# Performance work log

Hardware: AMD Instinct MI355X
Metric: run time of the kernel (lower is better)

## Reference

```python
import jax, jax.numpy as jnp
import numpy as np

HIDDEN = 1024
HEADS = 16
HEAD_DIM = HIDDEN // HEADS  # 64
BATCH = 2
SEQ = 2048
MASK_IDENTITY = True


def setup_inputs() -> dict:
    key = jax.random.key(0)
    ks = jax.random.split(key, 9)
    s = 1.0 / np.sqrt(HIDDEN)
    return {
        "hidden_states": jax.random.normal(ks[0], (BATCH, SEQ, HIDDEN), jnp.float32),
        "Wq": jax.random.normal(ks[1], (HIDDEN, HIDDEN), jnp.float32) * s,
        "bq": jnp.zeros((HIDDEN,), jnp.float32),
        "Wk": jax.random.normal(ks[2], (HIDDEN, HIDDEN), jnp.float32) * s,
        "bk": jnp.zeros((HIDDEN,), jnp.float32),
        "Wv": jax.random.normal(ks[3], (HIDDEN, HIDDEN), jnp.float32) * s,
        "bv": jnp.zeros((HIDDEN,), jnp.float32),
        "Wd": jax.random.normal(ks[4], (HIDDEN, HIDDEN), jnp.float32) * s,
        "bd": jnp.zeros((HIDDEN,), jnp.float32),
    }


def _split_heads(x):
    # [B, S, H*Dh] -> [B, H, S, Dh]
    b, s, _ = x.shape
    return x.reshape(b, s, HEADS, HEAD_DIM).transpose(0, 2, 1, 3)


def reference(hidden_states, Wq, bq, Wk, bk, Wv, bv, Wd, bd):
    # torch Linear: y = x @ W.T + b
    q = _split_heads(hidden_states @ Wq.T + bq)  # [B,H,S,Dh]
    k = _split_heads(hidden_states @ Wk.T + bk)
    v = _split_heads(hidden_states @ Wv.T + bv)

    scores = jnp.einsum("bhqd,bhkd->bhqk", q, k) / np.sqrt(HEAD_DIM)
    if MASK_IDENTITY:
        mask_value = -jnp.finfo(scores.dtype).max
        eye = jnp.eye(scores.shape[-1], dtype=bool)  # [S,S], broadcast over B,H
        scores = jnp.where(eye, mask_value, scores)
    probs = jax.nn.softmax(scores, axis=-1)
    ctx = jnp.einsum("bhqk,bhkd->bhqd", probs, v)  # [B,H,S,Dh]
    b, h, s, d = ctx.shape
    ctx = ctx.transpose(0, 2, 1, 3).reshape(b, s, h * d)  # [B,S,H*Dh]
    return ctx @ Wd.T + bd
```

## Files before the change

kernel.cpp:

```cpp
#include <hip/hip_runtime.h>
#include <hip/hip_bf16.h>
#include <stdint.h>

#define HIDDEN 1024
#define SEQL   2048
#define NB     2
#define NH     16
#define DH     64
#define MTOT   (NB * SEQL)
#define QKVLD  3072
#define SCALE_Q 0.18033688011112042f

typedef __bf16 bf16x8 __attribute__((ext_vector_type(8)));
typedef __bf16 bf16x4 __attribute__((ext_vector_type(4)));
typedef float  f32x4  __attribute__((ext_vector_type(4)));
typedef float  f32x16 __attribute__((ext_vector_type(16)));

__device__ __forceinline__ void gload16(const void* g, void* l) {
    __builtin_amdgcn_global_load_lds(
        (const __attribute__((address_space(1))) void*)g,
        (__attribute__((address_space(3))) void*)l, 16, 0, 0);
}
__device__ __forceinline__ float exp2fast(float x) {
    float r;
    asm("v_exp_f32 %0, %1" : "=v"(r) : "v"(x));
    return r;
}
__device__ __forceinline__ unsigned cvtpk(float lo, float hi) {
    unsigned r;
    asm("v_cvt_pk_bf16_f32 %0, %1, %2" : "=v"(r) : "v"(lo), "v"(hi));
    return r;
}
__device__ __forceinline__ void pswap(unsigned& a, unsigned& b) {
    asm volatile("v_permlane32_swap_b32 %0, %1" : "+v"(a), "+v"(b));
}

__global__ void cvt_f32_bf16(const float* __restrict__ src,
                             __bf16* __restrict__ dst, int n4) {
    int i = blockIdx.x * blockDim.x + threadIdx.x;
    if (i < n4) {
        float4 v = reinterpret_cast<const float4*>(src)[i];
        bf16x4 o = { (__bf16)v.x, (__bf16)v.y, (__bf16)v.z, (__bf16)v.w };
        reinterpret_cast<bf16x4*>(dst)[i] = o;
    }
}

__global__ void cvt_w4(const float* __restrict__ Wq, const float* __restrict__ Wk,
                       const float* __restrict__ Wv, const float* __restrict__ Wd,
                       __bf16* __restrict__ dst) {
    int seg = blockIdx.y;
    const float* src = seg == 0 ? Wq : seg == 1 ? Wk : seg == 2 ? Wv : Wd;
    float sc = (seg == 0) ? SCALE_Q : 1.0f;
    int i = blockIdx.x * 256 + threadIdx.x;
    float4 v = reinterpret_cast<const float4*>(src)[i];
    bf16x4 o = { (__bf16)(v.x * sc), (__bf16)(v.y * sc),
                 (__bf16)(v.z * sc), (__bf16)(v.w * sc) };
    reinterpret_cast<bf16x4*>(dst)[(size_t)seg * 262144 + i] = o;
}

__global__ void pack_bias(const float* __restrict__ bq, const float* __restrict__ bk,
                          const float* __restrict__ bv, float* __restrict__ dst) {
    int i = blockIdx.x * 256 + threadIdx.x;
    float v = (i < 1024) ? bq[i] * SCALE_Q : (i < 2048) ? bk[i - 1024] : bv[i - 2048];
    dst[i] = v;
}

__global__ __launch_bounds__(256) void transpose_v(const __bf16* __restrict__ QKV,
                                                   __bf16* __restrict__ Vt) {
    __shared__ __bf16 t[64][66];
    const int st = blockIdx.x, bh = blockIdx.y;
    const int b = bh >> 4, h = bh & 15;
    const int tid = threadIdx.x;
    const int r = tid >> 3, c = tid & 7;
    const __bf16* src = QKV + (size_t)(b * SEQL + st * 64) * QKVLD + 2048 + h * 64;
    *(int4*)&t[r][c * 8]      = *(const int4*)(src + (size_t)r * QKVLD + c * 8);
    *(int4*)&t[r + 32][c * 8] = *(const int4*)(src + (size_t)(r + 32) * QKVLD + c * 8);
    __syncthreads();
    __bf16* dst = Vt + (size_t)bh * DH * SEQL + st * 64;
    const int d = tid >> 3;
    __bf16 tmp0[8], tmp1[8];
#pragma unroll
    for (int j = 0; j < 8; ++j) {
        tmp0[j] = t[c * 8 + j][d];
        tmp1[j] = t[c * 8 + j][d + 32];
    }
    *(int4*)(dst + (size_t)d * SEQL + c * 8)        = *(int4*)tmp0;
    *(int4*)(dst + (size_t)(d + 32) * SEQL + c * 8) = *(int4*)tmp1;
}

__global__ __launch_bounds__(256) void gemm_qkv(const __bf16* __restrict__ A,
                                                const __bf16* __restrict__ Bw,
                                                const float* __restrict__ bias,
                                                __bf16* __restrict__ C) {
    __shared__ __bf16 As[128 * 32];
    __shared__ __bf16 Bs[128 * 32];
    const int K = 1024, N = QKVLD;

    int bid = blockIdx.x;
    int swz = (bid & 7) * 96 + (bid >> 3);
    const int bm = (swz & 31) * 128;
    const int bn = (swz >> 5) * 128;

    const int tid = threadIdx.x;
    const int w = tid >> 6, l = tid & 63, g = l >> 4, lc = l & 15;
    const int wr = (w >> 1) * 64, wc = (w & 1) * 64;
    const int row = tid >> 2, ch = tid & 3;

    const __bf16* Ap = A  + (size_t)(bm + row) * K + ch * 8;
    const __bf16* Bp = Bw + (size_t)(bn + row) * K + ch * 8;
    __bf16* AsLo = &As[w * 512];
    __bf16* AsHi = &As[2048 + w * 512];
    __bf16* BsLo = &Bs[w * 512];
    __bf16* BsHi = &Bs[2048 + w * 512];

    f32x4 acc[4][4];
    const f32x4 z4 = {0.f, 0.f, 0.f, 0.f};
#pragma unroll
    for (int i = 0; i < 4; ++i)
#pragma unroll
        for (int j = 0; j < 4; ++j) acc[i][j] = z4;

    for (int kt = 0; kt < K; kt += 32) {
        gload16(Ap + kt,                   AsLo);
        gload16(Ap + kt + (size_t)64 * K,  AsHi);
        gload16(Bp + kt,                   BsLo);
        gload16(Bp + kt + (size_t)64 * K,  BsHi);
        __syncthreads();

        bf16x8 af[4], bfr[4];
#pragma unroll
        for (int i = 0; i < 4; ++i)
            af[i] = *(const bf16x8*)&As[(wr + i * 16 + lc) * 32 + g * 8];
#pragma unroll
        for (int j = 0; j < 4; ++j)
            bfr[j] = *(const bf16x8*)&Bs[(wc + j * 16 + lc) * 32 + g * 8];
        __builtin_amdgcn_s_setprio(1);
#pragma unroll
        for (int i = 0; i < 4; ++i)
#pragma unroll
            for (int j = 0; j < 4; ++j)
                acc[i][j] = __builtin_amdgcn_mfma_f32_16x16x32_bf16(af[i], bfr[j], acc[i][j], 0, 0, 0);
        __builtin_amdgcn_s_setprio(0);
        __syncthreads();
    }

#pragma unroll
    for (int i = 0; i < 4; ++i) {
        int r0 = bm + wr + i * 16 + g * 4;
#pragma unroll
        for (int j = 0; j < 4; ++j) {
            int c = bn + wc + j * 16 + lc;
            float bb = bias[c];
#pragma unroll
            for (int r = 0; r < 4; ++r)
                C[(size_t)(r0 + r) * N + c] = (__bf16)(acc[i][j][r] + bb);
        }
    }
}

__global__ __launch_bounds__(256) void gemm_out(const __bf16* __restrict__ A,
                                                const __bf16* __restrict__ Bw,
                                                const float* __restrict__ bias,
                                                float* __restrict__ Cout) {
    __shared__ __bf16 As[128 * 32];
    __shared__ __bf16 Bs[128 * 32];
    const int M = MTOT, N = HIDDEN, K = HIDDEN;

    const int tid = threadIdx.x;
    const int w = tid >> 6, l = tid & 63, g = l >> 4, lc = l & 15;
    const int wr = (w >> 1) * 64, wc = (w & 1) * 64;
    const int bm = blockIdx.x * 128, bn = blockIdx.y * 128;
    const int row = tid >> 2, ch = tid & 3;

    const __bf16* Arow0 = A  + (size_t)(bm + row) * K + ch * 8;
    const __bf16* Arow1 = Arow0 + (size_t)64 * K;
    const __bf16* Brow0 = Bw + (size_t)(bn + row) * K + ch * 8;
    const __bf16* Brow1 = Brow0 + (size_t)64 * K;

    f32x4 acc[4][4];
    const f32x4 z4 = {0.f, 0.f, 0.f, 0.f};
#pragma unroll
    for (int i = 0; i < 4; ++i)
#pragma unroll
        for (int j = 0; j < 4; ++j) acc[i][j] = z4;

    int4 ra0 = *(const int4*)(Arow0);
    int4 ra1 = *(const int4*)(Arow1);
    int4 rb0 = *(const int4*)(Brow0);
    int4 rb1 = *(const int4*)(Brow1);

    for (int kt = 0; kt < K; kt += 32) {
        *(int4*)&As[row * 32 + ch * 8]        = ra0;
        *(int4*)&As[(64 + row) * 32 + ch * 8] = ra1;
        *(int4*)&Bs[row * 32 + ch * 8]        = rb0;
        *(int4*)&Bs[(64 + row) * 32 + ch * 8] = rb1;
        __syncthreads();

        if (kt + 32 < K) {
            ra0 = *(const int4*)(Arow0 + kt + 32);
            ra1 = *(const int4*)(Arow1 + kt + 32);
            rb0 = *(const int4*)(Brow0 + kt + 32);
            rb1 = *(const int4*)(Brow1 + kt + 32);
        }

        bf16x8 af[4], bfr[4];
#pragma unroll
        for (int i = 0; i < 4; ++i)
            af[i] = *(const bf16x8*)&As[(wr + i * 16 + lc) * 32 + g * 8];
#pragma unroll
        for (int j = 0; j < 4; ++j)
            bfr[j] = *(const bf16x8*)&Bs[(wc + j * 16 + lc) * 32 + g * 8];
        __builtin_amdgcn_s_setprio(1);
#pragma unroll
        for (int i = 0; i < 4; ++i)
#pragma unroll
            for (int j = 0; j < 4; ++j)
                acc[i][j] = __builtin_amdgcn_mfma_f32_16x16x32_bf16(af[i], bfr[j], acc[i][j], 0, 0, 0);
        __builtin_amdgcn_s_setprio(0);
        __syncthreads();
    }

#pragma unroll
    for (int i = 0; i < 4; ++i) {
        int r0 = bm + wr + i * 16 + g * 4;
#pragma unroll
        for (int j = 0; j < 4; ++j) {
            int c = bn + wc + j * 16 + lc;
            float bb = bias[c];
#pragma unroll
            for (int r = 0; r < 4; ++r)
                Cout[(size_t)(r0 + r) * N + c] = acc[i][j][r] + bb;
        }
    }
}

__global__ __launch_bounds__(256) void attn_kernel(const __bf16* __restrict__ QKV,
                                                   const __bf16* __restrict__ Vt,
                                                   __bf16* __restrict__ Ctx) {
    __shared__ __bf16 k_lds[2][64][64];
    __shared__ __bf16 v_lds[2][64][64];
    __shared__ float  bc[4][32];

    const int tid = threadIdx.x;
    const int w  = tid >> 6;
    const int l  = tid & 63;
    const int ql = l & 31;
    const int lh = l >> 5;

    int bid = blockIdx.x;
    int swz = (bid & 7) * 64 + (bid >> 3);
    const int qt = swz & 15, bh = swz >> 4;
    const int b = bh >> 4, hd = bh & 15;
    const int qw = qt * 128 + w * 32;

    const __bf16* Qg = QKV + (size_t)b * SEQL * QKVLD + hd * DH;
    const __bf16* Kg = Qg + 1024;
    const __bf16* Vg = Vt + (size_t)bh * DH * SEQL;

    bf16x8 qf[4];
    {
        const __bf16* qp = Qg + (size_t)(qw + ql) * QKVLD + lh * 8;
#pragma unroll
        for (int c = 0; c < 4; ++c) qf[c] = *(const bf16x8*)(qp + c * 16);
    }

    const int sr   = l >> 3;
    const int gcol = ((l & 7) * 8) ^ (sr << 3);
    auto stage = [&](int kb, int nb) {
        const __bf16* kp = Kg + (size_t)(kb + w * 8 + sr) * QKVLD + gcol;
        const __bf16* vp = Vg + (size_t)(w * 8 + sr) * SEQL + kb + gcol;
        gload16(kp,                          &k_lds[nb][w * 8][0]);
        gload16(kp + (size_t)32 * QKVLD,     &k_lds[nb][32 + w * 8][0]);
        gload16(vp,                          &v_lds[nb][w * 8][0]);
        gload16(vp + (size_t)32 * SEQL,      &v_lds[nb][32 + w * 8][0]);
    };

    stage(0, 0);
    __syncthreads();

    f32x16 o0, o1;
#pragma unroll
    for (int r = 0; r < 16; ++r) { o0[r] = 0.f; o1[r] = 0.f; }
    float m_r = -1e30f, l_r = 0.f;

    const int NT = SEQL / 64;
    const int rsw = (ql & 7) << 3;

    for (int kt = 0; kt < NT; ++kt) {
        const int buf = kt & 1;
        const int kb = kt * 64;

        if (kt + 1 < NT) stage(kb + 64, buf ^ 1);

        f32x16 sA, sB;
#pragma unroll
        for (int r = 0; r < 16; ++r) { sA[r] = 0.f; sB[r] = 0.f; }
        __builtin_amdgcn_s_setprio(1);
#pragma unroll
        for (int c = 0; c < 4; ++c) {
            bf16x8 k0 = *(const bf16x8*)&k_lds[buf][ql]     [(c * 16 + lh * 8) ^ rsw];
            bf16x8 k1 = *(const bf16x8*)&k_lds[buf][32 + ql][(c * 16 + lh * 8) ^ rsw];
            sA = __builtin_amdgcn_mfma_f32_32x32x16_bf16(k0, qf[c], sA, 0, 0, 0);
            sB = __builtin_amdgcn_mfma_f32_32x32x16_bf16(k1, qf[c], sB, 0, 0, 0);
        }
        __builtin_amdgcn_s_setprio(0);

        float p[32];
#pragma unroll
        for (int r = 0; r < 16; ++r) { p[r] = sA[r]; p[16 + r] = sB[r]; }

        if (kb < qw + 32 && qw < kb + 64) {
            const int qg = qw + ql;
#pragma unroll
            for (int i = 0; i < 32; ++i) {
                int kg = kb + ((i >> 4) << 5) + (i & 3) + ((i >> 2) & 3) * 8 + lh * 4;
                if (kg == qg) p[i] = -1e30f;
            }
        }

        float t16[16];
#pragma unroll
        for (int i = 0; i < 16; ++i) t16[i] = fmaxf(p[i], p[i + 16]);
#pragma unroll
        for (int i = 0; i < 8; ++i) t16[i] = fmaxf(t16[i], t16[i + 8]);
#pragma unroll
        for (int i = 0; i < 4; ++i) t16[i] = fmaxf(t16[i], t16[i + 4]);
        float pm = fmaxf(fmaxf(t16[0], t16[1]), fmaxf(t16[2], t16[3]));
        pm = fmaxf(pm, __shfl_xor(pm, 32, 64));

        if (__any(pm > m_r + 8.f)) {
            float mn = fmaxf(m_r, pm);
            float al = exp2fast(m_r - mn);
            m_r = mn;
            l_r *= al;
            if (lh == 0) bc[w][ql] = al;
            asm volatile("s_waitcnt lgkmcnt(0)" ::: "memory");
            float ag[16];
#pragma unroll
            for (int r = 0; r < 16; ++r)
                ag[r] = bc[w][(r & 3) + (r >> 2) * 8 + lh * 4];
#pragma unroll
            for (int r = 0; r < 16; ++r) { o0[r] *= ag[r]; o1[r] *= ag[r]; }
        }

#pragma unroll
        for (int i = 0; i < 32; ++i) p[i] = exp2fast(p[i] - m_r);
        float s16[16];
#pragma unroll
        for (int i = 0; i < 16; ++i) s16[i] = p[i] + p[i + 16];
#pragma unroll
        for (int i = 0; i < 8; ++i) s16[i] += s16[i + 8];
#pragma unroll
        for (int i = 0; i < 4; ++i) s16[i] += s16[i + 4];
        float rs = (s16[0] + s16[1]) + (s16[2] + s16[3]);
        rs += __shfl_xor(rs, 32, 64);
        l_r += rs;

        bf16x8 pa[4];
#pragma unroll
        for (int s = 0; s < 2; ++s) {
            unsigned w0 = cvtpk(p[s * 16 + 0],  p[s * 16 + 1]);
            unsigned w1 = cvtpk(p[s * 16 + 2],  p[s * 16 + 3]);
            unsigned w2 = cvtpk(p[s * 16 + 4],  p[s * 16 + 5]);
            unsigned w3 = cvtpk(p[s * 16 + 6],  p[s * 16 + 7]);
            unsigned w4 = cvtpk(p[s * 16 + 8],  p[s * 16 + 9]);
            unsigned w5 = cvtpk(p[s * 16 + 10], p[s * 16 + 11]);
            unsigned w6 = cvtpk(p[s * 16 + 12], p[s * 16 + 13]);
            unsigned w7 = cvtpk(p[s * 16 + 14], p[s * 16 + 15]);
            pswap(w0, w2); pswap(w1, w3);
            pswap(w4, w6); pswap(w5, w7);
            uint4 lo4 = {w0, w1, w2, w3};
            uint4 hi4 = {w4, w5, w6, w7};
            pa[s * 2 + 0] = *(bf16x8*)&lo4;
            pa[s * 2 + 1] = *(bf16x8*)&hi4;
        }

        __builtin_amdgcn_s_setprio(1);
#pragma unroll
        for (int s = 0; s < 2; ++s)
#pragma unroll
            for (int sl = 0; sl < 2; ++sl) {
                const int col = s * 32 + sl * 16 + lh * 8;
                bf16x8 v0 = *(const bf16x8*)&v_lds[buf][ql]     [col ^ rsw];
                bf16x8 v1 = *(const bf16x8*)&v_lds[buf][32 + ql][col ^ rsw];
                o0 = __builtin_amdgcn_mfma_f32_32x32x16_bf16(pa[s * 2 + sl], v0, o0, 0, 0, 0);
                o1 = __builtin_amdgcn_mfma_f32_32x32x16_bf16(pa[s * 2 + sl], v1, o1, 0, 0, 0);
            }
        __builtin_amdgcn_s_setprio(0);

        __syncthreads();
    }

    if (lh == 0) bc[w][ql] = 1.f / l_r;
    asm volatile("s_waitcnt lgkmcnt(0)" ::: "memory");
#pragma unroll
    for (int r = 0; r < 16; ++r) {
        int cr = (r & 3) + (r >> 2) * 8 + lh * 4;
        float iv = bc[w][cr];
        int qrow = qw + cr;
        __bf16* cp = Ctx + (size_t)(b * SEQL + qrow) * HIDDEN + hd * DH + ql;
        cp[0]  = (__bf16)(o0[r] * iv);
        cp[32] = (__bf16)(o1[r] * iv);
    }
}

extern "C" void kernel_launch(void* const* d_in, const int* in_sizes, int n_in,
                              void* d_out, int out_size, void* d_ws, size_t ws_size,
                              hipStream_t stream) {
    const float* H  = (const float*)d_in[0];
    const float* Wq = (const float*)d_in[1];
    const float* bq = (const float*)d_in[2];
    const float* Wk = (const float*)d_in[3];
    const float* bk = (const float*)d_in[4];
    const float* Wv = (const float*)d_in[5];
    const float* bv = (const float*)d_in[6];
    const float* Wd = (const float*)d_in[7];
    const float* bd = (const float*)d_in[8];
    float* out = (float*)d_out;

    char* ws = (char*)d_ws;
    const size_t MB = 1024 * 1024;
    __bf16* Hb    = (__bf16*)(ws + 0 * MB);
    __bf16* Ctx   = (__bf16*)(ws + 0 * MB);
    __bf16* Wqkvb = (__bf16*)(ws + 8 * MB);
    __bf16* Wdb   = (__bf16*)(ws + 14 * MB);
    float*  bqkv  = (float*) (ws + 16 * MB);
    __bf16* QKV   = (__bf16*)(ws + 17 * MB);
    __bf16* Vtb   = (__bf16*)(ws + 41 * MB);
    if (ws_size < 49 * MB) return;

    cvt_f32_bf16<<<4096, 256, 0, stream>>>(H, Hb, MTOT * HIDDEN / 4);
    cvt_w4<<<dim3(1024, 4), 256, 0, stream>>>(Wq, Wk, Wv, Wd, Wqkvb);
    pack_bias<<<12, 256, 0, stream>>>(bq, bk, bv, bqkv);

    gemm_qkv<<<768, 256, 0, stream>>>(Hb, Wqkvb, bqkv, QKV);

    transpose_v<<<dim3(32, 32), 256, 0, stream>>>(QKV, Vtb);

    attn_kernel<<<512, 256, 0, stream>>>(QKV, Vtb, Ctx);

    gemm_out<<<dim3(32, 8), 256, 0, stream>>>(Ctx, Wdb, bd, out);
}
```

Baseline: 137.4 us.

## Merge prep kernels, retile output GEMM with direct LDS loads, trim attention registers

The three preprocessing kernels (input cast, weight cast, bias pack) are merged into one launch to save launch overhead. The output projection GEMM moves from 128x128 to 64x128 tiles, giving 512 blocks instead of 256 for better CU occupancy. It also gets a swizzled block order and global_load_lds direct copies in place of register staging, which drops the register prefetch, so load and compute no longer overlap within a block. The attention kernel stops copying scores into a separate p array and seeds the first MFMA with a zero accumulator, reducing register pressure and VALU work.

After: 137.7 us. No clear change (+0.3%).

```diff
diff --git a/kernel.cpp b/kernel.cpp
--- a/kernel.cpp
+++ b/kernel.cpp
@@ -35,34 +35,36 @@
     asm volatile("v_permlane32_swap_b32 %0, %1" : "+v"(a), "+v"(b));
 }
 
-__global__ void cvt_f32_bf16(const float* __restrict__ src,
-                             __bf16* __restrict__ dst, int n4) {
-    int i = blockIdx.x * blockDim.x + threadIdx.x;
-    if (i < n4) {
+__global__ void prep(const float* __restrict__ H,
+                     const float* __restrict__ Wq, const float* __restrict__ Wk,
+                     const float* __restrict__ Wv, const float* __restrict__ Wd,
+                     const float* __restrict__ bq, const float* __restrict__ bk,
+                     const float* __restrict__ bv,
+                     __bf16* __restrict__ Hb, __bf16* __restrict__ Wall,
+                     float* __restrict__ bqkv) {
+    const int bid = blockIdx.x, tid = threadIdx.x;
+    if (bid < 4096) {
+        int i = bid * 256 + tid;
+        float4 v = reinterpret_cast<const float4*>(H)[i];
+        bf16x4 o = { (__bf16)v.x, (__bf16)v.y, (__bf16)v.z, (__bf16)v.w };
+        reinterpret_cast<bf16x4*>(Hb)[i] = o;
+    } else if (bid < 8192) {
+        int wi = bid - 4096;
+        int seg = wi >> 10;
+        int i = (wi & 1023) * 256 + tid;
+        const float* src = seg == 0 ? Wq : seg == 1 ? Wk : seg == 2 ? Wv : Wd;
+        float sc = (seg == 0) ? SCALE_Q : 1.0f;
         float4 v = reinterpret_cast<const float4*>(src)[i];
-        bf16x4 o = { (__bf16)v.x, (__bf16)v.y, (__bf16)v.z, (__bf16)v.w };
-        reinterpret_cast<bf16x4*>(dst)[i] = o;
-    }
-}
-
-__global__ void cvt_w4(const float* __restrict__ Wq, const float* __restrict__ Wk,
-                       const float* __restrict__ Wv, const float* __restrict__ Wd,
-                       __bf16* __restrict__ dst) {
-    int seg = blockIdx.y;
-    const float* src = seg == 0 ? Wq : seg == 1 ? Wk : seg == 2 ? Wv : Wd;
-    float sc = (seg == 0) ? SCALE_Q : 1.0f;
-    int i = blockIdx.x * 256 + threadIdx.x;
-    float4 v = reinterpret_cast<const float4*>(src)[i];
-    bf16x4 o = { (__bf16)(v.x * sc), (__bf16)(v.y * sc),
-                 (__bf16)(v.z * sc), (__bf16)(v.w * sc) };
-    reinterpret_cast<bf16x4*>(dst)[(size_t)seg * 262144 + i] = o;
-}
-
-__global__ void pack_bias(const float* __restrict__ bq, const float* __restrict__ bk,
-                          const float* __restrict__ bv, float* __restrict__ dst) {
-    int i = blockIdx.x * 256 + threadIdx.x;
-    float v = (i < 1024) ? bq[i] * SCALE_Q : (i < 2048) ? bk[i - 1024] : bv[i - 2048];
-    dst[i] = v;
+        bf16x4 o = { (__bf16)(v.x * sc), (__bf16)(v.y * sc),
+                     (__bf16)(v.z * sc), (__bf16)(v.w * sc) };
+        reinterpret_cast<bf16x4*>(Wall)[(size_t)seg * 262144 + i] = o;
+    } else {
+        for (int i = tid; i < 3072; i += 256) {
+            float v = (i < 1024) ? bq[i] * SCALE_Q
+                    : (i < 2048) ? bk[i - 1024] : bv[i - 2048];
+            bqkv[i] = v;
+        }
+    }
 }
 
 __global__ __launch_bounds__(256) void transpose_v(const __bf16* __restrict__ QKV,
@@ -162,57 +164,49 @@
                                                 const __bf16* __restrict__ Bw,
                                                 const float* __restrict__ bias,
                                                 float* __restrict__ Cout) {
-    __shared__ __bf16 As[128 * 32];
+    __shared__ __bf16 As[64 * 32];
     __shared__ __bf16 Bs[128 * 32];
-    const int M = MTOT, N = HIDDEN, K = HIDDEN;
+    const int K = 1024, N = 1024;
+
+    int bid = blockIdx.x;
+    int swz = (bid & 7) * 64 + (bid >> 3);
+    const int bm = (swz & 63) * 64;
+    const int bn = (swz >> 6) * 128;
 
     const int tid = threadIdx.x;
     const int w = tid >> 6, l = tid & 63, g = l >> 4, lc = l & 15;
-    const int wr = (w >> 1) * 64, wc = (w & 1) * 64;
-    const int bm = blockIdx.x * 128, bn = blockIdx.y * 128;
+    const int wr = (w >> 1) * 32, wc = (w & 1) * 64;
     const int row = tid >> 2, ch = tid & 3;
 
-    const __bf16* Arow0 = A  + (size_t)(bm + row) * K + ch * 8;
-    const __bf16* Arow1 = Arow0 + (size_t)64 * K;
-    const __bf16* Brow0 = Bw + (size_t)(bn + row) * K + ch * 8;
-    const __bf16* Brow1 = Brow0 + (size_t)64 * K;
-
-    f32x4 acc[4][4];
+    const __bf16* Ap = A  + (size_t)(bm + row) * K + ch * 8;
+    const __bf16* Bp = Bw + (size_t)(bn + row) * K + ch * 8;
+    __bf16* AsW  = &As[w * 512];
+    __bf16* BsLo = &Bs[w * 512];
+    __bf16* BsHi = &Bs[2048 + w * 512];
+
+    f32x4 acc[2][4];
     const f32x4 z4 = {0.f, 0.f, 0.f, 0.f};
 #pragma unroll
-    for (int i = 0; i < 4; ++i)
+    for (int i = 0; i < 2; ++i)
 #pragma unroll
         for (int j = 0; j < 4; ++j) acc[i][j] = z4;
 
-    int4 ra0 = *(const int4*)(Arow0);
-    int4 ra1 = *(const int4*)(Arow1);
-    int4 rb0 = *(const int4*)(Brow0);
-    int4 rb1 = *(const int4*)(Brow1);
-
     for (int kt = 0; kt < K; kt += 32) {
-        *(int4*)&As[row * 32 + ch * 8]        = ra0;
-        *(int4*)&As[(64 + row) * 32 + ch * 8] = ra1;
-        *(int4*)&Bs[row * 32 + ch * 8]        = rb0;
-        *(int4*)&Bs[(64 + row) * 32 + ch * 8] = rb1;
+        gload16(Ap + kt,                   AsW);
+        gload16(Bp + kt,                   BsLo);
+        gload16(Bp + kt + (size_t)64 * K,  BsHi);
         __syncthreads();
 
-        if (kt + 32 < K) {
-            ra0 = *(const int4*)(Arow0 + kt + 32);
-            ra1 = *(const int4*)(Arow1 + kt + 32);
-            rb0 = *(const int4*)(Brow0 + kt + 32);
-            rb1 = *(const int4*)(Brow1 + kt + 32);
-        }
-
-        bf16x8 af[4], bfr[4];
-#pragma unroll
-        for (int i = 0; i < 4; ++i)
+        bf16x8 af[2], bfr[4];
+#pragma unroll
+        for (int i = 0; i < 2; ++i)
             af[i] = *(const bf16x8*)&As[(wr + i * 16 + lc) * 32 + g * 8];
 #pragma unroll
         for (int j = 0; j < 4; ++j)
             bfr[j] = *(const bf16x8*)&Bs[(wc + j * 16 + lc) * 32 + g * 8];
         __builtin_amdgcn_s_setprio(1);
 #pragma unroll
-        for (int i = 0; i < 4; ++i)
+        for (int i = 0; i < 2; ++i)
 #pragma unroll
             for (int j = 0; j < 4; ++j)
                 acc[i][j] = __builtin_amdgcn_mfma_f32_16x16x32_bf16(af[i], bfr[j], acc[i][j], 0, 0, 0);
@@ -221,7 +215,7 @@
     }
 
 #pragma unroll
-    for (int i = 0; i < 4; ++i) {
+    for (int i = 0; i < 2; ++i) {
         int r0 = bm + wr + i * 16 + g * 4;
 #pragma unroll
         for (int j = 0; j < 4; ++j) {
@@ -283,6 +277,10 @@
     for (int r = 0; r < 16; ++r) { o0[r] = 0.f; o1[r] = 0.f; }
     float m_r = -1e30f, l_r = 0.f;
 
+    f32x16 zc;
+#pragma unroll
+    for (int r = 0; r < 16; ++r) zc[r] = 0.f;
+
     const int NT = SEQL / 64;
     const int rsw = (ql & 7) << 3;
 
@@ -293,11 +291,15 @@
         if (kt + 1 < NT) stage(kb + 64, buf ^ 1);
 
         f32x16 sA, sB;
-#pragma unroll
-        for (int r = 0; r < 16; ++r) { sA[r] = 0.f; sB[r] = 0.f; }
         __builtin_amdgcn_s_setprio(1);
-#pragma unroll
-        for (int c = 0; c < 4; ++c) {
+        {
+            bf16x8 k0 = *(const bf16x8*)&k_lds[buf][ql]     [(lh * 8) ^ rsw];
+            bf16x8 k1 = *(const bf16x8*)&k_lds[buf][32 + ql][(lh * 8) ^ rsw];
+            sA = __builtin_amdgcn_mfma_f32_32x32x16_bf16(k0, qf[0], zc, 0, 0, 0);
+            sB = __builtin_amdgcn_mfma_f32_32x32x16_bf16(k1, qf[0], zc, 0, 0, 0);
+        }
+#pragma unroll
+        for (int c = 1; c < 4; ++c) {
             bf16x8 k0 = *(const bf16x8*)&k_lds[buf][ql]     [(c * 16 + lh * 8) ^ rsw];
             bf16x8 k1 = *(const bf16x8*)&k_lds[buf][32 + ql][(c * 16 + lh * 8) ^ rsw];
             sA = __builtin_amdgcn_mfma_f32_32x32x16_bf16(k0, qf[c], sA, 0, 0, 0);
@@ -305,27 +307,23 @@
         }
         __builtin_amdgcn_s_setprio(0);
 
-        float p[32];
-#pragma unroll
-        for (int r = 0; r < 16; ++r) { p[r] = sA[r]; p[16 + r] = sB[r]; }
-
         if (kb < qw + 32 && qw < kb + 64) {
             const int qg = qw + ql;
 #pragma unroll
-            for (int i = 0; i < 32; ++i) {
-                int kg = kb + ((i >> 4) << 5) + (i & 3) + ((i >> 2) & 3) * 8 + lh * 4;
-                if (kg == qg) p[i] = -1e30f;
+            for (int i = 0; i < 16; ++i) {
+                int kg = kb + (i & 3) + ((i >> 2) & 3) * 8 + lh * 4;
+                if (kg == qg)      sA[i] = -1e30f;
+                if (kg + 32 == qg) sB[i] = -1e30f;
             }
         }
 
-        float t16[16];
-#pragma unroll
-        for (int i = 0; i < 16; ++i) t16[i] = fmaxf(p[i], p[i + 16]);
-#pragma unroll
-        for (int i = 0; i < 8; ++i) t16[i] = fmaxf(t16[i], t16[i + 8]);
-#pragma unroll
-        for (int i = 0; i < 4; ++i) t16[i] = fmaxf(t16[i], t16[i + 4]);
-        float pm = fmaxf(fmaxf(t16[0], t16[1]), fmaxf(t16[2], t16[3]));
+        float t8[8];
+#pragma unroll
+        for (int i = 0; i < 8; ++i)
+            t8[i] = fmaxf(fmaxf(sA[i], sA[i + 8]), fmaxf(sB[i], sB[i + 8]));
+#pragma unroll
+        for (int i = 0; i < 4; ++i) t8[i] = fmaxf(t8[i], t8[i + 4]);
+        float pm = fmaxf(fmaxf(t8[0], t8[1]), fmaxf(t8[2], t8[3]));
         pm = fmaxf(pm, __shfl_xor(pm, 32, 64));
 
         if (__any(pm > m_r + 8.f)) {
@@ -344,35 +342,51 @@
         }
 
 #pragma unroll
-        for (int i = 0; i < 32; ++i) p[i] = exp2fast(p[i] - m_r);
-        float s16[16];
-#pragma unroll
-        for (int i = 0; i < 16; ++i) s16[i] = p[i] + p[i + 16];
-#pragma unroll
-        for (int i = 0; i < 8; ++i) s16[i] += s16[i + 8];
-#pragma unroll
-        for (int i = 0; i < 4; ++i) s16[i] += s16[i + 4];
-        float rs = (s16[0] + s16[1]) + (s16[2] + s16[3]);
+        for (int i = 0; i < 16; ++i) sA[i] = exp2fast(sA[i] - m_r);
+#pragma unroll
+        for (int i = 0; i < 16; ++i) sB[i] = exp2fast(sB[i] - m_r);
+        float s8[8];
+#pragma unroll
+        for (int i = 0; i < 8; ++i)
+            s8[i] = (sA[i] + sA[i + 8]) + (sB[i] + sB[i + 8]);
+#pragma unroll
+        for (int i = 0; i < 4; ++i) s8[i] += s8[i + 4];
+        float rs = (s8[0] + s8[1]) + (s8[2] + s8[3]);
         rs += __shfl_xor(rs, 32, 64);
         l_r += rs;
 
         bf16x8 pa[4];
-#pragma unroll
-        for (int s = 0; s < 2; ++s) {
-            unsigned w0 = cvtpk(p[s * 16 + 0],  p[s * 16 + 1]);
-            unsigned w1 = cvtpk(p[s * 16 + 2],  p[s * 16 + 3]);
-            unsigned w2 = cvtpk(p[s * 16 + 4],  p[s * 16 + 5]);
-            unsigned w3 = cvtpk(p[s * 16 + 6],  p[s * 16 + 7]);
-            unsigned w4 = cvtpk(p[s * 16 + 8],  p[s * 16 + 9]);
-            unsigned w5 = cvtpk(p[s * 16 + 10], p[s * 16 + 11]);
-            unsigned w6 = cvtpk(p[s * 16 + 12], p[s * 16 + 13]);
-            unsigned w7 = cvtpk(p[s * 16 + 14], p[s * 16 + 15]);
+        {
+            unsigned w0 = cvtpk(sA[0],  sA[1]);
+            unsigned w1 = cvtpk(sA[2],  sA[3]);
+            unsigned w2 = cvtpk(sA[4],  sA[5]);
+            unsigned w3 = cvtpk(sA[6],  sA[7]);
+            unsigned w4 = cvtpk(sA[8],  sA[9]);
+            unsigned w5 = cvtpk(sA[10], sA[11]);
+            unsigned w6 = cvtpk(sA[12], sA[13]);
+            unsigned w7 = cvtpk(sA[14], sA[15]);
             pswap(w0, w2); pswap(w1, w3);
             pswap(w4, w6); pswap(w5, w7);
             uint4 lo4 = {w0, w1, w2, w3};
             uint4 hi4 = {w4, w5, w6, w7};
-            pa[s * 2 + 0] = *(bf16x8*)&lo4;
-            pa[s * 2 + 1] = *(bf16x8*)&hi4;
+            pa[0] = *(bf16x8*)&lo4;
+            pa[1] = *(bf16x8*)&hi4;
+        }
+        {
+            unsigned w0 = cvtpk(sB[0],  sB[1]);
+            unsigned w1 = cvtpk(sB[2],  sB[3]);
+            unsigned w2 = cvtpk(sB[4],  sB[5]);
+            unsigned w3 = cvtpk(sB[6],  sB[7]);
+            unsigned w4 = cvtpk(sB[8],  sB[9]);
+            unsigned w5 = cvtpk(sB[10], sB[11]);
+            unsigned w6 = cvtpk(sB[12], sB[13]);
+            unsigned w7 = cvtpk(sB[14], sB[15]);
+            pswap(w0, w2); pswap(w1, w3);
+            pswap(w4, w6); pswap(w5, w7);
+            uint4 lo4 = {w0, w1, w2, w3};
+            uint4 hi4 = {w4, w5, w6, w7};
+            pa[2] = *(bf16x8*)&lo4;
+            pa[3] = *(bf16x8*)&hi4;
         }
 
         __builtin_amdgcn_s_setprio(1);
@@ -429,9 +443,7 @@
     __bf16* Vtb   = (__bf16*)(ws + 41 * MB);
     if (ws_size < 49 * MB) return;
 
-    cvt_f32_bf16<<<4096, 256, 0, stream>>>(H, Hb, MTOT * HIDDEN / 4);
-    cvt_w4<<<dim3(1024, 4), 256, 0, stream>>>(Wq, Wk, Wv, Wd, Wqkvb);
-    pack_bias<<<12, 256, 0, stream>>>(bq, bk, bv, bqkv);
+    prep<<<8193, 256, 0, stream>>>(H, Wq, Wk, Wv, Wd, bq, bk, bv, Hb, Wqkvb, bqkv);
 
     gemm_qkv<<<768, 256, 0, stream>>>(Hb, Wqkvb, bqkv, QKV);
 
@@ -439,5 +451,5 @@
 
     attn_kernel<<<512, 256, 0, stream>>>(QKV, Vtb, Ctx);
 
-    gemm_out<<<dim3(32, 8), 256, 0, stream>>>(Ctx, Wdb, bd, out);
-}
+    gemm_out<<<512, 256, 0, stream>>>(Ctx, Wdb, bd, out);
+}
```
